# Kernel optimization log

Hardware: AMD Instinct MI355X
Metric: run time of the kernel (lower is better)

## Reference

```python
import jax, jax.numpy as jnp
import numpy as np

N_NODES = 100000
N_EDGES = 3200000
F_IN = 128
HID = 16
N_CLASSES = 32
N_RELS = 20
BN_EPS = 1e-5


def setup_inputs() -> dict:
    key = jax.random.key(0)
    ks = jax.random.split(key, 14)
    inp = {
        'x': jax.random.normal(ks[0], (N_NODES, F_IN), dtype=jnp.float32),
        'edge_index': jax.random.randint(ks[1], (2, N_EDGES), 0, N_NODES, dtype=jnp.int32),
        'edge_type': jax.random.randint(ks[2], (N_EDGES,), 0, N_RELS, dtype=jnp.int32),
        # conv1 params (relation weights, root weight, bias)
        'W1': jax.random.normal(ks[3], (N_RELS, F_IN, HID), dtype=jnp.float32) / np.sqrt(F_IN),
        'root1': jax.random.normal(ks[4], (F_IN, HID), dtype=jnp.float32) / np.sqrt(F_IN),
        'b1': jnp.zeros((HID,), dtype=jnp.float32),
        # bn1
        'gamma1': jnp.ones((HID,), dtype=jnp.float32),
        'beta1': jnp.zeros((HID,), dtype=jnp.float32),
        # conv2 params
        'W2': jax.random.normal(ks[5], (N_RELS, HID, N_CLASSES), dtype=jnp.float32) / np.sqrt(HID),
        'root2': jax.random.normal(ks[6], (HID, N_CLASSES), dtype=jnp.float32) / np.sqrt(HID),
        'b2': jnp.zeros((N_CLASSES,), dtype=jnp.float32),
        # bn2
        'gamma2': jnp.ones((N_CLASSES,), dtype=jnp.float32),
        'beta2': jnp.zeros((N_CLASSES,), dtype=jnp.float32),
    }
    return inp


def rgcn_conv(x, src, dst, etype, W, Wroot, b):
    # h[r] = x @ W_r  -> [R, N, O]; small O keeps this cheap
    h = jnp.einsum('nf,rfo->rno', x, W)
    msg = h[etype, src]  # [E, O] gather of transformed source features
    # per-(relation, dst-node) in-degree for mean aggregation
    cnt = jnp.zeros((W.shape[0], x.shape[0]), x.dtype).at[etype, dst].add(1.0)
    norm = jnp.where(cnt > 0, 1.0 / jnp.maximum(cnt, 1.0), 0.0)
    msg = msg * norm[etype, dst][:, None]
    out = jnp.zeros((x.shape[0], W.shape[-1]), x.dtype).at[dst].add(msg)
    return out + x @ Wroot + b


def batch_norm(x, gamma, beta):
    # training-mode BatchNorm1d: batch statistics, biased variance
    m = x.mean(axis=0)
    v = x.var(axis=0)
    return (x - m) * jax.lax.rsqrt(v + BN_EPS) * gamma + beta


def reference(x, edge_index, edge_type, W1, root1, b1, gamma1, beta1,
              W2, root2, b2, gamma2, beta2):
    src, dst = edge_index[0], edge_index[1]
    h = rgcn_conv(x, src, dst, edge_type, W1, root1, b1)
    h = jax.nn.relu(batch_norm(h, gamma1, beta1))
    # dropout(0.1) treated as identity (eval mode)
    h = rgcn_conv(h, src, dst, edge_type, W2, root2, b2)
    h = jax.nn.relu(batch_norm(h, gamma2, beta2))
    return jax.nn.log_softmax(h, axis=1)
```

## Files before the change

### kernel.cpp

```cpp
#include <hip/hip_runtime.h>
#include <hip/hip_bf16.h>

#define N_NODES 100000
#define N_EDGES 3200000
#define F_IN 128
#define HID 16
#define N_CLASSES 32
#define N_RELS 20
#define BN_EPS 1e-5f
#define N_CELLS (N_NODES * N_RELS)
#define BIN_SHIFT 13
#define BIN_CELLS 8192
#define NBINS ((N_CELLS + BIN_CELLS - 1) / BIN_CELLS)
#define CHUNK 8192
#define NBLK ((N_EDGES + CHUNK - 1) / CHUNK)
#define HM_N (NBINS * NBLK)
#define HM_NB ((HM_N + 2047) / 2048)
#define SLOT_ELEMS (N_NODES * HID)
#define XPAD 136

#define OFF_CS     0ull
#define OFF_REC    8000000ull
#define OFF_AGG1   20800000ull
#define OFF_HM     27200000ull
#define OFF_BSUM   27584000ull
#define OFF_BINOFF 27588096ull
#define OFF_ST1    27589120ull
#define OFF_ST2    27589376ull
#define OFF_WT     27589632ull
#define OFF_W2T    27675648ull
#define OFF_X      27698176ull
#define SLOT_BYTES 3200000ull

typedef __attribute__((ext_vector_type(8))) short bf16x8;
typedef __attribute__((ext_vector_type(4))) short bf16x4;
typedef __attribute__((ext_vector_type(4))) float f32x4;

__device__ inline short f2bf(float f) {
    union { __hip_bfloat16 h; short s; } u;
    u.h = __float2bfloat16(f);
    return u.s;
}

__device__ inline float bf2f(short s) {
    union { unsigned u; float f; } x;
    x.u = ((unsigned)(unsigned short)s) << 16;
    return x.f;
}


__global__ __launch_bounds__(256) void hist2_kernel(const int* __restrict__ et,
                                                    const int* __restrict__ dst,
                                                    int* __restrict__ hm) {
    __shared__ int lh[NBINS];
    int t = threadIdx.x;
    for (int i = t; i < NBINS; i += 256) lh[i] = 0;
    __syncthreads();
    int e0 = blockIdx.x * CHUNK, e1 = min(e0 + CHUNK, N_EDGES);
    for (int e = e0 + t; e < e1; e += 256) {
        int m = et[e] * N_NODES + dst[e];
        atomicAdd(&lh[m >> BIN_SHIFT], 1);
    }
    __syncthreads();
    for (int i = t; i < NBINS; i += 256) hm[i * NBLK + blockIdx.x] = lh[i];
}

__global__ void scan_k1(const int* __restrict__ a, int* __restrict__ bsum, int n) {
    __shared__ int red[256];
    int base = blockIdx.x * 2048 + threadIdx.x * 8;
    int s = 0;
#pragma unroll
    for (int i = 0; i < 8; ++i) {
        int idx = base + i;
        if (idx < n) s += a[idx];
    }
    red[threadIdx.x] = s;
    __syncthreads();
    for (int off = 128; off > 0; off >>= 1) {
        if (threadIdx.x < off) red[threadIdx.x] += red[threadIdx.x + off];
        __syncthreads();
    }
    if (threadIdx.x == 0) bsum[blockIdx.x] = red[0];
}

__global__ void scan_k2(int* __restrict__ bsum, int nb) {
    __shared__ int p[1024];
    int t = threadIdx.x;
    int v = (t < nb) ? bsum[t] : 0;
    p[t] = v;
    __syncthreads();
    for (int off = 1; off < 1024; off <<= 1) {
        int a = (t >= off) ? p[t - off] : 0;
        __syncthreads();
        p[t] += a;
        __syncthreads();
    }
    if (t < nb) bsum[t] = p[t] - v;
}

__global__ void scan_k3(int* __restrict__ a, const int* __restrict__ bsum, int n) {
    __shared__ int red[256];
    int base = blockIdx.x * 2048 + threadIdx.x * 8;
    int v[8];
    int s = 0;
#pragma unroll
    for (int i = 0; i < 8; ++i) {
        int idx = base + i;
        v[i] = (idx < n) ? a[idx] : 0;
        s += v[i];
    }
    red[threadIdx.x] = s;
    __syncthreads();
    for (int off = 1; off < 256; off <<= 1) {
        int t = (threadIdx.x >= off) ? red[threadIdx.x - off] : 0;
        __syncthreads();
        red[threadIdx.x] += t;
        __syncthreads();
    }
    int run = bsum[blockIdx.x] + red[threadIdx.x] - s;
#pragma unroll
    for (int i = 0; i < 8; ++i) {
        int idx = base + i;
        if (idx < n) a[idx] = run;
        run += v[i];
    }
}

__global__ void binoff_kernel(const int* __restrict__ hm, int* __restrict__ binoff) {
    int t = threadIdx.x;
    if (t < NBINS) binoff[t] = hm[t * NBLK];
    if (t == 0) binoff[NBINS] = N_EDGES;
}

__global__ __launch_bounds__(256) void bucket2_kernel(const int* __restrict__ src,
                                                      const int* __restrict__ dst,
                                                      const int* __restrict__ et,
                                                      const int* __restrict__ hm,
                                                      unsigned* __restrict__ bucket) {
    __shared__ int ptr[NBINS];
    int t = threadIdx.x;
    for (int i = t; i < NBINS; i += 256) ptr[i] = hm[i * NBLK + blockIdx.x];
    __syncthreads();
    int e0 = blockIdx.x * CHUNK, e1 = min(e0 + CHUNK, N_EDGES);
    for (int e = e0 + t; e < e1; e += 256) {
        int m = et[e] * N_NODES + dst[e];
        int pos = atomicAdd(&ptr[m >> BIN_SHIFT], 1);
        bucket[pos] = ((unsigned)(m & (BIN_CELLS - 1)) << 17) | (unsigned)src[e];
    }
}

__global__ __launch_bounds__(256) void place_kernel(const unsigned* __restrict__ bucket,
                                                    const int* __restrict__ binoff,
                                                    int* __restrict__ cs,
                                                    unsigned* __restrict__ rec) {
    __shared__ int cnt[BIN_CELLS];
    __shared__ int part[256];
    int b = blockIdx.x;
    int cellbase = b << BIN_SHIFT;
    int ncells = min(BIN_CELLS, N_CELLS - cellbase);
    int ebase = binoff[b], eend = binoff[b + 1];
    int t = threadIdx.x;
    for (int i = t; i < BIN_CELLS; i += 256) cnt[i] = 0;
    __syncthreads();
    for (int e = ebase + t; e < eend; e += 256) {
        int c = (int)(bucket[e] >> 17);
        atomicAdd(&cnt[c], 1);
    }
    __syncthreads();
    int b32 = t * 32;
    int s = 0;
#pragma unroll
    for (int i = 0; i < 32; ++i) s += cnt[b32 + i];
    part[t] = s;
    __syncthreads();
    for (int off = 1; off < 256; off <<= 1) {
        int a = (t >= off) ? part[t - off] : 0;
        __syncthreads();
        part[t] += a;
        __syncthreads();
    }
    int run = (t ? part[t - 1] : 0);
#pragma unroll
    for (int i = 0; i < 32; ++i) { int c = cnt[b32 + i]; cnt[b32 + i] = run; run += c; }
    __syncthreads();
    for (int e = ebase + t; e < eend; e += 256) {
        unsigned p = bucket[e];
        int c = (int)(p >> 17);
        int pos = ebase + atomicAdd(&cnt[c], 1);
        rec[pos] = p & 0x1FFFFu;
    }
    __syncthreads();
    for (int c = t; c < ncells; c += 256) cs[cellbase + c] = ebase + cnt[c];
}


__global__ void wt_convert(const float* __restrict__ W1, const float* __restrict__ root1,
                           __hip_bfloat16* __restrict__ Wt) {
    int r = blockIdx.x;
    const float* src = (r < N_RELS) ? (W1 + (size_t)r * F_IN * HID) : root1;
    for (int i = threadIdx.x; i < F_IN * HID; i += 256) {
        int f = i >> 4, o = i & 15;
        int s = f >> 5, kgrp = (f >> 3) & 3, e = f & 7;
        size_t dst = (((size_t)(r * 4 + s) * 64) + kgrp * 16 + o) * 8 + e;
        Wt[dst] = __float2bfloat16(src[i]);
    }
}

__global__ void wt2_convert(const float* __restrict__ W2, const float* __restrict__ root2,
                            __hip_bfloat16* __restrict__ W2t) {
    int i = blockIdx.x * 256 + threadIdx.x;
    if (i < 11 * 32 * 32) {
        int p = i >> 10, oc = (i >> 5) & 31, k = i & 31;
        float v;
        if (p == 10) v = (k < 16) ? root2[k * N_CLASSES + oc] : 0.f;
        else v = W2[((size_t)(2 * p + (k >> 4)) * HID + (k & 15)) * N_CLASSES + oc];
        W2t[i] = __float2bfloat16(v);
    }
}


__global__ __launch_bounds__(256, 4) void xform_gemm(const float* __restrict__ x,
                                                     const __hip_bfloat16* __restrict__ Wt,
                                                     const float* __restrict__ b1,
                                                     __hip_bfloat16* __restrict__ h1,
                                                     float* __restrict__ agg1) {
    __shared__ __hip_bfloat16 xs[64 * XPAD];
    int t = threadIdx.x;
    int nodeBase = blockIdx.x * 64;

#pragma unroll
    for (int it = 0; it < 4; ++it) {
        int idx = it * 256 + t;
        int ln = idx >> 4;
        int g = (idx & 15) * 8;
        int node = nodeBase + ln;
        float4 a = {0.f, 0.f, 0.f, 0.f}, b = {0.f, 0.f, 0.f, 0.f};
        if (node < N_NODES) {
            const float* xp = x + (size_t)node * F_IN + g;
            a = *(const float4*)xp;
            b = *(const float4*)(xp + 4);
        }
        bf16x8 v;
        v[0] = f2bf(a.x); v[1] = f2bf(a.y); v[2] = f2bf(a.z); v[3] = f2bf(a.w);
        v[4] = f2bf(b.x); v[5] = f2bf(b.y); v[6] = f2bf(b.z); v[7] = f2bf(b.w);
        *(bf16x8*)(&xs[ln * XPAD + g]) = v;
    }
    __syncthreads();

    int lane = t & 63;
    int wave = t >> 6;
    int col = lane & 15;
    int kgrp = lane >> 4;
    int row = wave * 16 + col;
    int node = nodeBase + row;
    bool valid = node < N_NODES;

    bf16x8 xf[4];
#pragma unroll
    for (int s = 0; s < 4; ++s)
        xf[s] = *(const bf16x8*)(&xs[row * XPAD + s * 32 + kgrp * 8]);

    for (int r = 0; r < N_RELS + 1; ++r) {
        f32x4 acc = {0.f, 0.f, 0.f, 0.f};
#pragma unroll
        for (int s = 0; s < 4; ++s) {
            bf16x8 wf = *(const bf16x8*)(Wt + (((size_t)(r * 4 + s) * 64) + lane) * 8);
            acc = __builtin_amdgcn_mfma_f32_16x16x32_bf16(wf, xf[s], acc, 0, 0, 0);
        }
        if (valid) {
            if (r < N_RELS) {
                union { ushort4 u4; short s4[4]; } o;
                o.s4[0] = f2bf(acc[0]); o.s4[1] = f2bf(acc[1]);
                o.s4[2] = f2bf(acc[2]); o.s4[3] = f2bf(acc[3]);
                *(ushort4*)(h1 + ((size_t)r * N_NODES + node) * HID + kgrp * 4) = o.u4;
            } else {
                int c0 = kgrp * 4;
                float4 o = {acc[0] + b1[c0], acc[1] + b1[c0 + 1],
                            acc[2] + b1[c0 + 2], acc[3] + b1[c0 + 3]};
                *(float4*)(agg1 + (size_t)node * HID + c0) = o;
            }
        }
    }
}

__global__ __launch_bounds__(256) void conv1_agg(const __hip_bfloat16* __restrict__ h1,
                                                 const unsigned* __restrict__ rec,
                                                 const int* __restrict__ cs,
                                                 float* __restrict__ agg1,
                                                 float* __restrict__ st1) {
    __shared__ float ls[HID], lq[HID];
    if (threadIdx.x < HID) { ls[threadIdx.x] = 0.f; lq[threadIdx.x] = 0.f; }
    __syncthreads();
    int q = threadIdx.x & 3, slot = threadIdx.x >> 2;
    int d = blockIdx.x * 64 + slot;
    bool valid = d < N_NODES;
    int dd = valid ? d : 0;
    float acc[4] = {0.f, 0.f, 0.f, 0.f};

    for (int rb = 0; rb < N_RELS; rb += 4) {
        int s0v[4], s1v[4];
#pragma unroll
        for (int j = 0; j < 4; ++j) {
            int m = (rb + j) * N_NODES + dd;
            s0v[j] = (m == 0) ? 0 : cs[m - 1];
            s1v[j] = cs[m];
        }
#pragma unroll
        for (int j = 0; j < 4; ++j) {
            int s0 = s0v[j], s1 = s1v[j];
            if (s1 > s0) {
                const __hip_bfloat16* hr = h1 + (size_t)(rb + j) * SLOT_ELEMS + q * 4;
                float pa[4] = {0.f, 0.f, 0.f, 0.f};
                for (int i = s0; i < s1; ++i) {
                    int sn = rec[i];
                    bf16x4 v = *(const bf16x4*)(hr + (size_t)sn * HID);
#pragma unroll
                    for (int k = 0; k < 4; ++k) pa[k] += bf2f(v[k]);
                }
                float inv = 1.0f / (float)(s1 - s0);
#pragma unroll
                for (int k = 0; k < 4; ++k) acc[k] = fmaf(pa[k], inv, acc[k]);
            }
        }
    }

    float vout[4] = {0.f, 0.f, 0.f, 0.f};
    if (valid) {
        float4* ap = (float4*)(agg1 + (size_t)d * HID + q * 4);
        float4 a0 = *ap;
        vout[0] = a0.x + acc[0]; vout[1] = a0.y + acc[1];
        vout[2] = a0.z + acc[2]; vout[3] = a0.w + acc[3];
        *ap = float4{vout[0], vout[1], vout[2], vout[3]};
    }
#pragma unroll
    for (int k = 0; k < 4; ++k) {
        atomicAdd(&ls[q * 4 + k], vout[k]);
        atomicAdd(&lq[q * 4 + k], vout[k] * vout[k]);
    }
    __syncthreads();
    if (threadIdx.x < HID) {
        atomicAdd(&st1[threadIdx.x], ls[threadIdx.x]);
        atomicAdd(&st1[HID + threadIdx.x], lq[threadIdx.x]);
    }
}

__global__ void bn_relu1(const float* __restrict__ a, const float* __restrict__ stats,
                         const float* __restrict__ gamma, const float* __restrict__ beta,
                         __hip_bfloat16* __restrict__ hb) {
    int i = blockIdx.x * 256 + threadIdx.x;
    if (i < N_NODES * HID) {
        int j = i & (HID - 1);
        float mean = stats[j] * (1.0f / N_NODES);
        float var = stats[HID + j] * (1.0f / N_NODES) - mean * mean;
        float rs = rsqrtf(var + BN_EPS);
        float val = (a[i] - mean) * rs * gamma[j] + beta[j];
        hb[i] = __float2bfloat16(fmaxf(val, 0.f));
    }
}


__global__ __launch_bounds__(256) void conv2_agg(const __hip_bfloat16* __restrict__ hbnb,
                                                 const unsigned* __restrict__ rec,
                                                 const int* __restrict__ cs,
                                                 __hip_bfloat16* __restrict__ agg2) {
    int pair = threadIdx.x >> 1, half = threadIdx.x & 1;
    int m = blockIdx.x * 128 + pair;
    if (m >= N_CELLS) return;
    int s0 = (m == 0) ? 0 : cs[m - 1];
    int s1 = cs[m];
    const __hip_bfloat16* hb = hbnb + half * 8;
    float acc[8] = {0.f, 0.f, 0.f, 0.f, 0.f, 0.f, 0.f, 0.f};
    for (int i = s0; i < s1; ++i) {
        int sn = rec[i];
        bf16x8 v = *(const bf16x8*)(hb + (size_t)sn * HID);
#pragma unroll
        for (int k = 0; k < 8; ++k) acc[k] += bf2f(v[k]);
    }
    float inv = (s1 > s0) ? 1.0f / (float)(s1 - s0) : 0.f;
    bf16x8 o;
#pragma unroll
    for (int k = 0; k < 8; ++k) o[k] = f2bf(acc[k] * inv);
    *(bf16x8*)(agg2 + (size_t)m * HID + half * 8) = o;
}

__global__ __launch_bounds__(256) void gemm2(const __hip_bfloat16* __restrict__ agg2,
                                             const __hip_bfloat16* __restrict__ W2t,
                                             const float* __restrict__ b2,
                                             float* __restrict__ buf2) {
    int wave = threadIdx.x >> 6, lane = threadIdx.x & 63;
    int col = lane & 15, kgrp = lane >> 4;
    int node = blockIdx.x * 64 + wave * 16 + col;
    bool valid = node < N_NODES;
    int nidx = valid ? node : 0;

    bf16x8 bf[11];
#pragma unroll
    for (int p = 0; p < 11; ++p) {
        int slot = 2 * p + (kgrp >> 1);
        bf[p] = *(const bf16x8*)(agg2 + ((size_t)slot * N_NODES + nidx) * HID + (kgrp & 1) * 8);
    }
#pragma unroll
    for (int ct = 0; ct < 2; ++ct) {
        f32x4 acc = {0.f, 0.f, 0.f, 0.f};
#pragma unroll
        for (int p = 0; p < 11; ++p) {
            bf16x8 wf = *(const bf16x8*)(W2t + ((size_t)p * 32 + ct * 16 + col) * 32 + kgrp * 8);
            acc = __builtin_amdgcn_mfma_f32_16x16x32_bf16(wf, bf[p], acc, 0, 0, 0);
        }
        if (valid) {
            int c0 = ct * 16 + kgrp * 4;
            float4 o = {acc[0] + b2[c0], acc[1] + b2[c0 + 1],
                        acc[2] + b2[c0 + 2], acc[3] + b2[c0 + 3]};
            *(float4*)(buf2 + (size_t)node * N_CLASSES + c0) = o;
        }
    }
}

template <int CH>
__global__ void bn_stats(const float* __restrict__ v, float* __restrict__ stats) {
    __shared__ float ls[CH], lq[CH];
    if (threadIdx.x < CH) { ls[threadIdx.x] = 0.f; lq[threadIdx.x] = 0.f; }
    __syncthreads();
    const int total = N_NODES * CH;
    int j = threadIdx.x % CH;
    float s = 0.f, q = 0.f;
    for (int i = blockIdx.x * blockDim.x + threadIdx.x; i < total; i += gridDim.x * blockDim.x) {
        float t = v[i];
        s += t; q += t * t;
    }
    atomicAdd(&ls[j], s);
    atomicAdd(&lq[j], q);
    __syncthreads();
    if (threadIdx.x < CH) {
        atomicAdd(&stats[threadIdx.x], ls[threadIdx.x]);
        atomicAdd(&stats[CH + threadIdx.x], lq[threadIdx.x]);
    }
}

__global__ void final_kernel(const float* __restrict__ buf2, const float* __restrict__ stats,
                             const float* __restrict__ gamma, const float* __restrict__ beta,
                             float* __restrict__ out) {
    int idx = blockIdx.x * 256 + threadIdx.x;
    int j = threadIdx.x & 31;
    float mean = stats[j] * (1.0f / N_NODES);
    float var = stats[N_CLASSES + j] * (1.0f / N_NODES) - mean * mean;
    float rs = rsqrtf(var + BN_EPS);
    float v = fmaxf((buf2[idx] - mean) * rs * gamma[j] + beta[j], 0.f);
    float m = v;
#pragma unroll
    for (int o = 16; o >= 1; o >>= 1) m = fmaxf(m, __shfl_xor(m, o, 32));
    float ex = __expf(v - m);
    float ssum = ex;
#pragma unroll
    for (int o = 16; o >= 1; o >>= 1) ssum += __shfl_xor(ssum, o, 32);
    out[idx] = (v - m) - logf(ssum);
}

extern "C" void kernel_launch(void* const* d_in, const int* in_sizes, int n_in,
                              void* d_out, int out_size, void* d_ws, size_t ws_size,
                              hipStream_t stream) {
    const float* x      = (const float*)d_in[0];
    const int*   eidx   = (const int*)d_in[1];
    const int*   etype  = (const int*)d_in[2];
    const float* W1     = (const float*)d_in[3];
    const float* root1  = (const float*)d_in[4];
    const float* b1     = (const float*)d_in[5];
    const float* gamma1 = (const float*)d_in[6];
    const float* beta1  = (const float*)d_in[7];
    const float* W2     = (const float*)d_in[8];
    const float* root2  = (const float*)d_in[9];
    const float* b2     = (const float*)d_in[10];
    const float* gamma2 = (const float*)d_in[11];
    const float* beta2  = (const float*)d_in[12];

    const int* src = eidx;
    const int* dst = eidx + N_EDGES;

    char* ws = (char*)d_ws;
    int*      cs     = (int*)(ws + OFF_CS);
    unsigned* rec    = (unsigned*)(ws + OFF_REC);
    float*    buf2   = (float*)(ws + OFF_REC);
    float*    agg1   = (float*)(ws + OFF_AGG1);
    int*      hm     = (int*)(ws + OFF_HM);
    int*      bsum   = (int*)(ws + OFF_BSUM);
    int*      binoff = (int*)(ws + OFF_BINOFF);
    float*    st1    = (float*)(ws + OFF_ST1);
    float*    st2    = (float*)(ws + OFF_ST2);
    __hip_bfloat16* Wt  = (__hip_bfloat16*)(ws + OFF_WT);
    __hip_bfloat16* W2t = (__hip_bfloat16*)(ws + OFF_W2T);
    unsigned* bucket = (unsigned*)(ws + OFF_X);
    __hip_bfloat16* rx   = (__hip_bfloat16*)(ws + OFF_X);
    __hip_bfloat16* h1   = rx;
    __hip_bfloat16* hbnb = rx + (size_t)20 * SLOT_ELEMS;
    __hip_bfloat16* agg2 = rx;

    float* out = (float*)d_out;

    hipMemsetAsync(st1, 0, 512, stream);

    hist2_kernel<<<NBLK, 256, 0, stream>>>(etype, dst, hm);
    scan_k1<<<HM_NB, 256, 0, stream>>>(hm, bsum, HM_N);
    scan_k2<<<1, 1024, 0, stream>>>(bsum, HM_NB);
    scan_k3<<<HM_NB, 256, 0, stream>>>(hm, bsum, HM_N);
    binoff_kernel<<<1, 256, 0, stream>>>(hm, binoff);
    bucket2_kernel<<<NBLK, 256, 0, stream>>>(src, dst, etype, hm, bucket);
    place_kernel<<<NBINS, 256, 0, stream>>>(bucket, binoff, cs, rec);

    wt_convert<<<N_RELS + 1, 256, 0, stream>>>(W1, root1, Wt);
    wt2_convert<<<(11 * 32 * 32 + 255) / 256, 256, 0, stream>>>(W2, root2, W2t);

    xform_gemm<<<(N_NODES + 63) / 64, 256, 0, stream>>>(x, Wt, b1, h1, agg1);

    conv1_agg<<<(N_NODES + 63) / 64, 256, 0, stream>>>(h1, rec, cs, agg1, st1);
    bn_relu1<<<(N_NODES * HID + 255) / 256, 256, 0, stream>>>(agg1, st1, gamma1, beta1, hbnb);

    conv2_agg<<<(N_CELLS + 127) / 128, 256, 0, stream>>>(hbnb, rec, cs, agg2);
    gemm2<<<(N_NODES + 63) / 64, 256, 0, stream>>>(agg2, W2t, b2, buf2);
    bn_stats<N_CLASSES><<<512, 256, 0, stream>>>(buf2, st2);
    final_kernel<<<(N_NODES * N_CLASSES + 255) / 256, 256, 0, stream>>>(buf2, st2, gamma2, beta2, out);
}
```

Measured before the change: 314.2 us.

## Fuse conv2 aggregation, GEMM and BN stats into one kernel via LDS

Merges the per-relation mean aggregation, the MFMA transform and the BN2 statistics into a single kernel. Each block aggregates the neighbor features of 64 destination nodes across all relations into shared memory, then runs the MFMA from LDS. This removes the round trip of the 20-slot agg2 buffer through global memory and the separate pass that re-reads buf2 for statistics. In exchange, each thread now walks edge lists serially across four relations with narrower 4-element loads, which lowers parallelism in the gather phase, and the per-element shared atomics add contention.

```diff
diff --git a/kernel.cpp b/kernel.cpp
--- a/kernel.cpp
+++ b/kernel.cpp
@@ -359,45 +359,72 @@
 }
 
 
-__global__ __launch_bounds__(256) void conv2_agg(const __hip_bfloat16* __restrict__ hbnb,
-                                                 const unsigned* __restrict__ rec,
-                                                 const int* __restrict__ cs,
-                                                 __hip_bfloat16* __restrict__ agg2) {
-    int pair = threadIdx.x >> 1, half = threadIdx.x & 1;
-    int m = blockIdx.x * 128 + pair;
-    if (m >= N_CELLS) return;
-    int s0 = (m == 0) ? 0 : cs[m - 1];
-    int s1 = cs[m];
-    const __hip_bfloat16* hb = hbnb + half * 8;
-    float acc[8] = {0.f, 0.f, 0.f, 0.f, 0.f, 0.f, 0.f, 0.f};
-    for (int i = s0; i < s1; ++i) {
-        int sn = rec[i];
-        bf16x8 v = *(const bf16x8*)(hb + (size_t)sn * HID);
-#pragma unroll
-        for (int k = 0; k < 8; ++k) acc[k] += bf2f(v[k]);
-    }
-    float inv = (s1 > s0) ? 1.0f / (float)(s1 - s0) : 0.f;
-    bf16x8 o;
-#pragma unroll
-    for (int k = 0; k < 8; ++k) o[k] = f2bf(acc[k] * inv);
-    *(bf16x8*)(agg2 + (size_t)m * HID + half * 8) = o;
-}
-
-__global__ __launch_bounds__(256) void gemm2(const __hip_bfloat16* __restrict__ agg2,
-                                             const __hip_bfloat16* __restrict__ W2t,
-                                             const float* __restrict__ b2,
-                                             float* __restrict__ buf2) {
-    int wave = threadIdx.x >> 6, lane = threadIdx.x & 63;
+__global__ __launch_bounds__(256) void conv2_fused(const __hip_bfloat16* __restrict__ hbnb,
+                                                   const unsigned* __restrict__ rec,
+                                                   const int* __restrict__ cs,
+                                                   const __hip_bfloat16* __restrict__ W2t,
+                                                   const float* __restrict__ b2,
+                                                   float* __restrict__ buf2,
+                                                   float* __restrict__ st2) {
+    __shared__ __hip_bfloat16 ms[22 * 64 * 16];
+    __shared__ float ls[N_CLASSES], lq[N_CLASSES];
+    int t = threadIdx.x;
+    if (t < N_CLASSES) { ls[t] = 0.f; lq[t] = 0.f; }
+    *(bf16x4*)(&ms[21 * 64 * 16 + t * 4]) = bf16x4{0, 0, 0, 0};
+
+    int q = t & 3, slotd = t >> 2;
+    int d = blockIdx.x * 64 + slotd;
+    bool valid = d < N_NODES;
+    int dd = valid ? d : 0;
+
+    {
+        bf16x4 hv = *(const bf16x4*)(hbnb + (size_t)dd * HID + q * 4);
+        *(bf16x4*)(&ms[(20 * 64 + slotd) * 16 + q * 4]) = hv;
+    }
+
+    for (int rb = 0; rb < N_RELS; rb += 4) {
+        int s0v[4], s1v[4];
+#pragma unroll
+        for (int j = 0; j < 4; ++j) {
+            int m = (rb + j) * N_NODES + dd;
+            s0v[j] = (m == 0) ? 0 : cs[m - 1];
+            s1v[j] = cs[m];
+        }
+#pragma unroll
+        for (int j = 0; j < 4; ++j) {
+            int s0 = s0v[j], s1 = s1v[j];
+            float pa[4] = {0.f, 0.f, 0.f, 0.f};
+            if (s1 > s0) {
+                const __hip_bfloat16* hb = hbnb + q * 4;
+                for (int i = s0; i < s1; ++i) {
+                    int sn = rec[i];
+                    bf16x4 v = *(const bf16x4*)(hb + (size_t)sn * HID);
+#pragma unroll
+                    for (int k = 0; k < 4; ++k) pa[k] += bf2f(v[k]);
+                }
+                float inv = 1.0f / (float)(s1 - s0);
+#pragma unroll
+                for (int k = 0; k < 4; ++k) pa[k] *= inv;
+            }
+            bf16x4 o;
+#pragma unroll
+            for (int k = 0; k < 4; ++k) o[k] = f2bf(pa[k]);
+            *(bf16x4*)(&ms[((rb + j) * 64 + slotd) * 16 + q * 4]) = o;
+        }
+    }
+    __syncthreads();
+
+    int wave = t >> 6, lane = t & 63;
     int col = lane & 15, kgrp = lane >> 4;
-    int node = blockIdx.x * 64 + wave * 16 + col;
-    bool valid = node < N_NODES;
-    int nidx = valid ? node : 0;
+    int ln = wave * 16 + col;
+    int node = blockIdx.x * 64 + ln;
+    bool valid2 = node < N_NODES;
 
     bf16x8 bf[11];
 #pragma unroll
     for (int p = 0; p < 11; ++p) {
         int slot = 2 * p + (kgrp >> 1);
-        bf[p] = *(const bf16x8*)(agg2 + ((size_t)slot * N_NODES + nidx) * HID + (kgrp & 1) * 8);
+        bf[p] = *(const bf16x8*)(&ms[(slot * 64 + ln) * 16 + (kgrp & 1) * 8]);
     }
 #pragma unroll
     for (int ct = 0; ct < 2; ++ct) {
@@ -407,33 +434,22 @@
             bf16x8 wf = *(const bf16x8*)(W2t + ((size_t)p * 32 + ct * 16 + col) * 32 + kgrp * 8);
             acc = __builtin_amdgcn_mfma_f32_16x16x32_bf16(wf, bf[p], acc, 0, 0, 0);
         }
-        if (valid) {
+        if (valid2) {
             int c0 = ct * 16 + kgrp * 4;
-            float4 o = {acc[0] + b2[c0], acc[1] + b2[c0 + 1],
-                        acc[2] + b2[c0 + 2], acc[3] + b2[c0 + 3]};
-            *(float4*)(buf2 + (size_t)node * N_CLASSES + c0) = o;
-        }
-    }
-}
-
-template <int CH>
-__global__ void bn_stats(const float* __restrict__ v, float* __restrict__ stats) {
-    __shared__ float ls[CH], lq[CH];
-    if (threadIdx.x < CH) { ls[threadIdx.x] = 0.f; lq[threadIdx.x] = 0.f; }
-    __syncthreads();
-    const int total = N_NODES * CH;
-    int j = threadIdx.x % CH;
-    float s = 0.f, q = 0.f;
-    for (int i = blockIdx.x * blockDim.x + threadIdx.x; i < total; i += gridDim.x * blockDim.x) {
-        float t = v[i];
-        s += t; q += t * t;
-    }
-    atomicAdd(&ls[j], s);
-    atomicAdd(&lq[j], q);
-    __syncthreads();
-    if (threadIdx.x < CH) {
-        atomicAdd(&stats[threadIdx.x], ls[threadIdx.x]);
-        atomicAdd(&stats[CH + threadIdx.x], lq[threadIdx.x]);
+            float v0[4];
+#pragma unroll
+            for (int k = 0; k < 4; ++k) {
+                v0[k] = acc[k] + b2[c0 + k];
+                atomicAdd(&ls[c0 + k], v0[k]);
+                atomicAdd(&lq[c0 + k], v0[k] * v0[k]);
+            }
+            *(float4*)(buf2 + (size_t)node * N_CLASSES + c0) = float4{v0[0], v0[1], v0[2], v0[3]};
+        }
+    }
+    __syncthreads();
+    if (t < N_CLASSES) {
+        atomicAdd(&st2[t], ls[t]);
+        atomicAdd(&st2[N_CLASSES + t], lq[t]);
     }
 }
 
@@ -479,7 +495,6 @@
     char* ws = (char*)d_ws;
     int*      cs     = (int*)(ws + OFF_CS);
     unsigned* rec    = (unsigned*)(ws + OFF_REC);
-    float*    buf2   = (float*)(ws + OFF_REC);
     float*    agg1   = (float*)(ws + OFF_AGG1);
     int*      hm     = (int*)(ws + OFF_HM);
     int*      bsum   = (int*)(ws + OFF_BSUM);
@@ -492,7 +507,7 @@
     __hip_bfloat16* rx   = (__hip_bfloat16*)(ws + OFF_X);
     __hip_bfloat16* h1   = rx;
     __hip_bfloat16* hbnb = rx + (size_t)20 * SLOT_ELEMS;
-    __hip_bfloat16* agg2 = rx;
+    float*    buf2   = (float*)(ws + OFF_X);
 
     float* out = (float*)d_out;
 
@@ -514,8 +529,6 @@
     conv1_agg<<<(N_NODES + 63) / 64, 256, 0, stream>>>(h1, rec, cs, agg1, st1);
     bn_relu1<<<(N_NODES * HID + 255) / 256, 256, 0, stream>>>(agg1, st1, gamma1, beta1, hbnb);
 
-    conv2_agg<<<(N_CELLS + 127) / 128, 256, 0, stream>>>(hbnb, rec, cs, agg2);
-    gemm2<<<(N_NODES + 63) / 64, 256, 0, stream>>>(agg2, W2t, b2, buf2);
-    bn_stats<N_CLASSES><<<512, 256, 0, stream>>>(buf2, st2);
+    conv2_fused<<<(N_NODES + 63) / 64, 256, 0, stream>>>(hbnb, rec, cs, W2t, b2, buf2, st2);
     final_kernel<<<(N_NODES * N_CLASSES + 255) / 256, 256, 0, stream>>>(buf2, st2, gamma2, beta2, out);
 }
```

Measured after the change: 402.6 us. +28.1%, slower.
